# Kernel optimization log

Measured on AMD Instinct MI355X. Metric: run time of the kernel, lower is better.

Reference implementation:

```python
import jax, jax.numpy as jnp
import numpy as np

EPS = 1e-9
# exp factors for iterations i = 4,3,2,1,0,-1,-2 ; i == -2 -> 0.0
EXP_FACTORS = np.array([-(4.0 ** i) if i != -2 else 0.0 for i in range(4, -3, -1)], dtype=np.float32)


def setup_inputs() -> dict:
    key = jax.random.key(0)
    k1, k2 = jax.random.split(key)
    B, N, D = 16, 2048, 256
    preds = jax.random.normal(k1, (B, N, D), dtype=jnp.float32)
    labels = jax.random.normal(k2, (B, N, D), dtype=jnp.float32)
    return {"preds": preds, "labels": labels}


def _pairwise_dist(p1, p2):
    # [B,N,1] + [B,1,N] - 2 * p1 @ p2^T -> [B,N,N]
    p1_norm = jnp.sum(p1 * p1, axis=-1)[..., :, None]
    p2_norm = jnp.sum(p2 * p2, axis=-1)[..., None, :]
    return p1_norm + p2_norm - 2.0 * jnp.einsum('bnd,bmd->bnm', p1, p2)


def _approx_match(pwdist):
    B, N, _ = pwdist.shape
    match0 = jnp.zeros_like(pwdist)
    currency0 = jnp.ones((B, N, 1), dtype=pwdist.dtype)
    cost0 = jnp.ones((B, 1, N), dtype=pwdist.dtype)

    def body(carry, exp_factor):
        match, cost, currency = carry
        bids = jnp.exp(exp_factor * pwdist) * cost              # [B,N,N]
        bids = bids * currency / (jnp.sum(bids, axis=2, keepdims=True) + EPS)
        bid_wt = jnp.minimum(cost / (jnp.sum(bids, axis=1, keepdims=True) + EPS), 1.0)
        bids = bids * bid_wt
        match = match + bids
        cost = jnp.maximum(cost - jnp.sum(bids, axis=1, keepdims=True), 0.0)
        currency = jnp.maximum(currency - jnp.sum(bids, axis=2, keepdims=True), 0.0)
        return (match, cost, currency), None

    (match, _, _), _ = jax.lax.scan(body, (match0, cost0, currency0), jnp.asarray(EXP_FACTORS))
    return match


def reference(preds, labels):
    pwdist = _pairwise_dist(preds, labels)
    match = _approx_match(pwdist)
    return jnp.sum(match * pwdist)
```

## Files before the change

### kernel.cpp

```cpp
#include <hip/hip_runtime.h>
#include <cstdint>

#define B_ 16
#define N_ 2048
#define D_ 256
#define EPS_ 1e-9f

#define AS1 __attribute__((address_space(1)))
#define AS3 __attribute__((address_space(3)))

typedef float f4 __attribute__((ext_vector_type(4)));
typedef __attribute__((ext_vector_type(8))) short short8;

__device__ inline unsigned short f2bf(float x){
  unsigned int u = __float_as_uint(x);
  u = (u + 0x7fffu + ((u >> 16) & 1u)) >> 16;
  return (unsigned short)u;
}
__device__ inline float bf2f(unsigned short u){
  return __uint_as_float(((unsigned int)u) << 16);
}

__device__ float blockReduceSum(float x, float* red){
  int tid = threadIdx.x;
  red[tid] = x; __syncthreads();
  #pragma unroll
  for (int off = 128; off > 0; off >>= 1){
    if (tid < off) red[tid] += red[tid + off];
    __syncthreads();
  }
  float r = red[0]; __syncthreads();
  return r;
}

__global__ __launch_bounds__(256) void prep_kernel(
    const float* __restrict__ preds, const float* __restrict__ labels,
    unsigned short* __restrict__ pabf, unsigned short* __restrict__ pbbf,
    float* __restrict__ pn, float* __restrict__ ln,
    float* __restrict__ cost, float* __restrict__ currency,
    int* __restrict__ dmin, float* __restrict__ PL,
    float* __restrict__ scal, float* __restrict__ out){
  int s = blockIdx.y;
  int tid = threadIdx.x;
  if (s == 0){
    int i = blockIdx.x * 256 + tid;
    if (i < B_ * N_){ cost[i] = 1.f; currency[i] = 1.f; }
    if (i < 2 * B_ * D_) PL[i] = 0.f;
    if (i < B_ * 4) scal[i] = 0.f;
    if (i < B_) dmin[i] = 0x7f7fffff;
    if (i == 0) out[0] = 0.f;
  }
  const float* src = s ? labels : preds;
  unsigned short* dst = s ? pbbf : pabf;
  float* norms = s ? ln : pn;
  int wid = (blockIdx.x * 256 + tid) >> 6;
  int lane = tid & 63;
  size_t row0 = (size_t)wid * 4;
  float4 v[4];
  #pragma unroll
  for (int q = 0; q < 4; q++)
    v[q] = ((const float4*)(src + (row0 + q) * D_))[lane];
  #pragma unroll
  for (int q = 0; q < 4; q++){
    float sum = v[q].x*v[q].x + v[q].y*v[q].y + v[q].z*v[q].z + v[q].w*v[q].w;
    #pragma unroll
    for (int off = 32; off >= 1; off >>= 1) sum += __shfl_xor(sum, off);
    if (lane == 0) norms[row0 + q] = sum;
    ushort4 o; o.x = f2bf(v[q].x); o.y = f2bf(v[q].y); o.z = f2bf(v[q].z); o.w = f2bf(v[q].w);
    ((ushort4*)(dst + (row0 + q) * D_))[lane] = o;
  }
}

__global__ __launch_bounds__(512) void gemm_minmax(
    const unsigned short* __restrict__ pa, const unsigned short* __restrict__ pbm,
    const float* __restrict__ pn, const float* __restrict__ ln,
    int* __restrict__ dmin)
{
  int lid = blockIdx.x;
  int xcd = lid & 7, sq = lid >> 3;
  int b = 2 * xcd + (sq >> 4);
  int rest = sq & 15;
  int tm = (rest >> 1) * 256;
  int tnh = rest & 1;
  const unsigned short* A  = pa  + (size_t)b * N_ * D_;
  const unsigned short* Bm = pbm + (size_t)b * N_ * D_;
  __shared__ __align__(16) unsigned short As[2][256 * 64];
  __shared__ __align__(16) unsigned short Bs[2][256 * 64];
  __shared__ float minred[8];
  int tid = threadIdx.x, lane = tid & 63, w = tid >> 6;
  int wm = (w >> 2) * 128, wn = (w & 3) * 64;
  int quad = lane >> 4, l15 = lane & 15;

  f4 acc[8][4];
  #pragma unroll
  for (int i = 0; i < 8; i++)
    #pragma unroll
    for (int j = 0; j < 4; j++) acc[i][j] = (f4)0.f;

  int lr = lane >> 3, ch = lane & 7;
  int gch = (ch ^ lr) * 8;

  auto load_stage = [&](int st){
    int ti = st >> 2, ki = st & 3;
    int tn = (tnh * 4 + ti) * 256;
    int kt = ki * 64;
    int bufI = st & 1;
    #pragma unroll
    for (int p = 0; p < 4; p++){
      int R = p * 64 + w * 8;
      int r = R + lr;
      __builtin_amdgcn_global_load_lds(
          (const AS1 unsigned int*)(const void*)&A[(size_t)(tm + r) * D_ + kt + gch],
          (AS3 unsigned int*)(void*)&As[bufI][R * 64], 16, 0, 0);
      __builtin_amdgcn_global_load_lds(
          (const AS1 unsigned int*)(const void*)&Bm[(size_t)(tn + r) * D_ + kt + gch],
          (AS3 unsigned int*)(void*)&Bs[bufI][R * 64], 16, 0, 0);
    }
  };

  load_stage(0);
  float lnr[4];
  float mind = 3.4e38f;
  for (int st = 0; st < 16; st++){
    __syncthreads();
    if (st < 15) load_stage(st + 1);
    int ki = st & 3;
    if (ki == 0){
      int tn = (tnh * 4 + (st >> 2)) * 256;
      #pragma unroll
      for (int jj = 0; jj < 4; jj++)
        lnr[jj] = ln[(size_t)b * N_ + tn + wn + jj * 16 + l15];
    }
    int buf = st & 1;
    #pragma unroll
    for (int ks = 0; ks < 2; ks++){
      short8 af[8], bf[4];
      int j = ks * 4 + quad;
      #pragma unroll
      for (int i = 0; i < 8; i++){
        int ra = wm + i * 16 + l15;
        af[i] = *(const short8*)(&As[buf][ra * 64 + ((j ^ (ra & 7)) * 8)]);
      }
      #pragma unroll
      for (int jj = 0; jj < 4; jj++){
        int rb = wn + jj * 16 + l15;
        bf[jj] = *(const short8*)(&Bs[buf][rb * 64 + ((j ^ (rb & 7)) * 8)]);
      }
      #pragma unroll
      for (int i = 0; i < 8; i++)
        #pragma unroll
        for (int jj = 0; jj < 4; jj++)
          acc[i][jj] = __builtin_amdgcn_mfma_f32_16x16x32_bf16(af[i], bf[jj], acc[i][jj], 0, 0, 0);
    }
    if (ki == 3){
      #pragma unroll
      for (int i = 0; i < 8; i++){
        float4 pv4 = *(const float4*)&pn[(size_t)b * N_ + tm + wm + i * 16 + quad * 4];
        float pv[4] = {pv4.x, pv4.y, pv4.z, pv4.w};
        #pragma unroll
        for (int jj = 0; jj < 4; jj++){
          #pragma unroll
          for (int reg = 0; reg < 4; reg++){
            float v = pv[reg] + lnr[jj] - 2.f * acc[i][jj][reg];
            mind = fminf(mind, v);
            acc[i][jj][reg] = 0.f;
          }
        }
      }
    }
  }

  #pragma unroll
  for (int off = 32; off >= 1; off >>= 1) mind = fminf(mind, __shfl_xor(mind, off));
  if (lane == 0) minred[w] = mind;
  __syncthreads();
  if (tid == 0){
    float m = minred[0];
    #pragma unroll
    for (int q = 1; q < 8; q++) m = fminf(m, minred[q]);
    atomicMin(&dmin[b], __float_as_int(fmaxf(m, 0.f)));
  }
}

__global__ __launch_bounds__(256) void fb_all(
    const unsigned short* __restrict__ pabf, const unsigned short* __restrict__ pbbf,
    const float* __restrict__ pn, const float* __restrict__ ln,
    float* __restrict__ cost, float* __restrict__ currency,
    const int* __restrict__ dmin, float* __restrict__ out,
    float* __restrict__ alpha, float* __restrict__ v, float* __restrict__ scal)
{
  const float EF[6] = {-256.f, -64.f, -16.f, -4.f, -1.f, -0.25f};
  int b = blockIdx.x, tid = threadIdx.x;
  float dm = __int_as_float(dmin[b]);
  __shared__ float red[256];
  __shared__ float alpha_l[N_];
  __shared__ float prow[D_];
  const unsigned short* A  = pabf + (size_t)b * N_ * D_;
  const unsigned short* Bm = pbbf + (size_t)b * N_ * D_;
  const float* pnb = pn + (size_t)b * N_;
  const float* lnb = ln + (size_t)b * N_;
  float* costb = cost + (size_t)b * N_;
  float* curb  = currency + (size_t)b * N_;
  for (int it = 0; it < 6; it++){
    float ef = EF[it];
    if (ef * (dm - 8.f) < -55.f) continue;
    float cost_c[8], colsum_c[8], bw_c[8], costnew_c[8];
    #pragma unroll
    for (int j = 0; j < 8; j++){ cost_c[j] = costb[j*256+tid]; colsum_c[j] = 0.f; }
    for (int r = 0; r < N_; r++){
      prow[tid] = bf2f(A[(size_t)r * D_ + tid]);
      __syncthreads();
      float s_c[8], rs = 0.f;
      for (int j = 0; j < 8; j++){
        int m = j*256+tid; float dot = 0.f;
        for (int k = 0; k < D_; k++) dot += prow[k] * bf2f(Bm[(size_t)m * D_ + k]);
        float d = pnb[r] + lnb[m] - 2.f*dot;
        float s = __expf(ef * d) * cost_c[j];
        s_c[j] = s; rs += s;
      }
      float tot = blockReduceSum(rs, red);
      float a = curb[r] / (tot + EPS_);
      if (tid == 0) alpha_l[r] = a;
      #pragma unroll
      for (int j = 0; j < 8; j++) colsum_c[j] += s_c[j] * a;
      __syncthreads();
    }
    #pragma unroll
    for (int j = 0; j < 8; j++){
      float cs = colsum_c[j];
      float bw = fminf(cost_c[j] / (cs + EPS_), 1.f);
      bw_c[j] = bw; costnew_c[j] = fmaxf(cost_c[j] - bw*cs, 0.f);
    }
    float contrib = 0.f;
    for (int r = 0; r < N_; r++){
      prow[tid] = bf2f(A[(size_t)r * D_ + tid]);
      __syncthreads();
      float a = alpha_l[r], rbs = 0.f;
      for (int j = 0; j < 8; j++){
        int m = j*256+tid; float dot = 0.f;
        for (int k = 0; k < D_; k++) dot += prow[k] * bf2f(Bm[(size_t)m * D_ + k]);
        float d = pnb[r] + lnb[m] - 2.f*dot;
        float bid = __expf(ef * d) * cost_c[j] * a * bw_c[j];
        rbs += bid; contrib += bid * d;
      }
      float tot = blockReduceSum(rbs, red);
      if (tid == 0) curb[r] = fmaxf(curb[r] - tot, 0.f);
      __syncthreads();
    }
    #pragma unroll
    for (int j = 0; j < 8; j++) costb[j*256+tid] = costnew_c[j];
    float ctot = blockReduceSum(contrib, red);
    if (tid == 0) atomicAdd(out, ctot);
    __syncthreads();
  }
  float* ab = alpha + (size_t)b * N_;
  float* vb = v + (size_t)b * N_;
  float s = 0.f;
  #pragma unroll
  for (int j = 0; j < 8; j++) s += costb[j*256+tid];
  float Sc = blockReduceSum(s, red);
  float sa = 0.f, spn = 0.f;
  #pragma unroll
  for (int j = 0; j < 8; j++){
    int i = j*256+tid;
    float a = curb[i] / (Sc + EPS_);
    ab[i] = a; sa += a; spn += a * pnb[i];
  }
  float Sa  = blockReduceSum(sa, red);
  float Spn = blockReduceSum(spn, red);
  float sv = 0.f, sln = 0.f;
  #pragma unroll
  for (int j = 0; j < 8; j++){
    int i = j*256+tid;
    float c = costb[j*256+tid];
    float bw = fminf(c / (c * Sa + EPS_), 1.f);
    float vv = c * bw;
    vb[i] = vv; sv += vv; sln += vv * lnb[i];
  }
  float Sv  = blockReduceSum(sv, red);
  float Sln = blockReduceSum(sln, red);
  if (tid == 0){
    scal[b*4+0] = Sa; scal[b*4+1] = Sv; scal[b*4+2] = Spn; scal[b*4+3] = Sln;
  }
}

__global__ __launch_bounds__(256) void cf_wsum(
    const unsigned short* __restrict__ pabf, const unsigned short* __restrict__ pbbf,
    const float* __restrict__ alpha, const float* __restrict__ v,
    float* __restrict__ PL)
{
  int chunk = blockIdx.x, src = blockIdx.y, b = blockIdx.z, tid = threadIdx.x;
  int g = tid >> 6, c4 = (tid & 63) * 4;
  const unsigned short* X = (src ? pbbf : pabf) + ((size_t)b * N_ + chunk * 64) * D_;
  const float* wv = (src ? v : alpha) + (size_t)b * N_ + chunk * 64;
  __shared__ float wl[64];
  __shared__ float part[4][D_];
  if (tid < 64) wl[tid] = wv[tid];
  __syncthreads();
  f4 acc = (f4)0.f;
  for (int r = g * 16; r < g * 16 + 16; r++){
    uint2 pk = *(const uint2*)&X[(size_t)r * D_ + c4];
    float wr = wl[r];
    acc[0] = fmaf(wr, __uint_as_float(pk.x << 16), acc[0]);
    acc[1] = fmaf(wr, __uint_as_float(pk.x & 0xffff0000u), acc[1]);
    acc[2] = fmaf(wr, __uint_as_float(pk.y << 16), acc[2]);
    acc[3] = fmaf(wr, __uint_as_float(pk.y & 0xffff0000u), acc[3]);
  }
  #pragma unroll
  for (int q = 0; q < 4; q++) part[g][c4 + q] = acc[q];
  __syncthreads();
  float s = part[0][tid] + part[1][tid] + part[2][tid] + part[3][tid];
  atomicAdd(&PL[((size_t)src * B_ + b) * D_ + tid], s);
}

__global__ __launch_bounds__(256) void cf_final(
    const float* __restrict__ PL, const float* __restrict__ scal,
    float* __restrict__ out)
{
  int b = blockIdx.x, tid = threadIdx.x;
  __shared__ float red[256];
  float p = PL[(size_t)b * D_ + tid] * PL[((size_t)B_ + b) * D_ + tid];
  float dot = blockReduceSum(p, red);
  if (tid == 0){
    float Sa = scal[b*4+0], Sv = scal[b*4+1], Spn = scal[b*4+2], Sln = scal[b*4+3];
    atomicAdd(out, Spn * Sv + Sa * Sln - 2.f * dot);
  }
}

extern "C" void kernel_launch(void* const* d_in, const int* in_sizes, int n_in,
                              void* d_out, int out_size, void* d_ws, size_t ws_size,
                              hipStream_t stream)
{
  const float* preds  = (const float*)d_in[0];
  const float* labels = (const float*)d_in[1];
  float* out = (float*)d_out;
  char* ws = (char*)d_ws;
  const size_t BN = (size_t)B_ * N_;
  size_t off = 0;
  float* cost     = (float*)(ws + off); off += BN * 4;
  float* currency = (float*)(ws + off); off += BN * 4;
  float* alpha    = (float*)(ws + off); off += BN * 4;
  float* v        = (float*)(ws + off); off += BN * 4;
  float* pn       = (float*)(ws + off); off += BN * 4;
  float* ln       = (float*)(ws + off); off += BN * 4;
  int*   dmin     = (int*)(ws + off);   off += 256;
  float* scal     = (float*)(ws + off); off += 256;
  float* PL       = (float*)(ws + off); off += (size_t)2 * B_ * D_ * 4;
  unsigned short* pabf = (unsigned short*)(ws + off); off += BN * D_ * 2;
  unsigned short* pbbf = (unsigned short*)(ws + off); off += BN * D_ * 2;

  prep_kernel<<<dim3((unsigned)(BN / 16), 2), 256, 0, stream>>>(
      preds, labels, pabf, pbbf, pn, ln, cost, currency, dmin, PL, scal, out);
  gemm_minmax<<<dim3(256), 512, 0, stream>>>(pabf, pbbf, pn, ln, dmin);
  fb_all<<<dim3(B_), 256, 0, stream>>>(pabf, pbbf, pn, ln, cost, currency, dmin, out,
                                       alpha, v, scal);
  cf_wsum<<<dim3(32, 2, B_), 256, 0, stream>>>(pabf, pbbf, alpha, v, PL);
  cf_final<<<dim3(B_), 256, 0, stream>>>(PL, scal, out);
}
```

Measured before the change: 152.4 us.

## Retile min-distance GEMM into smaller 256x128 tiles across more blocks

Retiles the pairwise-distance min-reduction GEMM from 256 persistent blocks, each sweeping four 256x256 output tiles, to 2048 blocks that each own one 256x128 tile with K-steps of 32. The LDS layout is reswizzled to pack two 32-wide rows per 64-element line, and the accumulator array is halved so up to four blocks can be resident per CU. This aims to raise occupancy and latency hiding on a GEMM that left most CUs underused. In exchange, operands are reloaded more often and there are more block launches and atomics.

Measured after the change: 157.1 us. 1.03x slower.

```diff
diff --git a/kernel.cpp b/kernel.cpp
--- a/kernel.cpp
+++ b/kernel.cpp
@@ -71,105 +71,108 @@
   }
 }
 
-__global__ __launch_bounds__(512) void gemm_minmax(
+__global__ __launch_bounds__(512, 4) void gemm_minmax(
     const unsigned short* __restrict__ pa, const unsigned short* __restrict__ pbm,
     const float* __restrict__ pn, const float* __restrict__ ln,
     int* __restrict__ dmin)
 {
   int lid = blockIdx.x;
   int xcd = lid & 7, sq = lid >> 3;
-  int b = 2 * xcd + (sq >> 4);
-  int rest = sq & 15;
-  int tm = (rest >> 1) * 256;
-  int tnh = rest & 1;
+  int b = 2 * xcd + (sq >> 7);
+  int t = sq & 127;
+  int tm = (t & 7) * 256;
+  int tn = (t >> 3) * 128;
   const unsigned short* A  = pa  + (size_t)b * N_ * D_;
   const unsigned short* Bm = pbm + (size_t)b * N_ * D_;
-  __shared__ __align__(16) unsigned short As[2][256 * 64];
-  __shared__ __align__(16) unsigned short Bs[2][256 * 64];
+  __shared__ __align__(16) unsigned short As[2][256 * 32];
+  __shared__ __align__(16) unsigned short Bs[2][128 * 32];
   __shared__ float minred[8];
   int tid = threadIdx.x, lane = tid & 63, w = tid >> 6;
-  int wm = (w >> 2) * 128, wn = (w & 3) * 64;
+  int wm = (w >> 1) * 64, wn = (w & 1) * 64;
   int quad = lane >> 4, l15 = lane & 15;
-
-  f4 acc[8][4];
-  #pragma unroll
-  for (int i = 0; i < 8; i++)
+  int l8 = lane >> 3, c7 = lane & 7;
+
+  f4 acc[4][4];
+  #pragma unroll
+  for (int i = 0; i < 4; i++)
     #pragma unroll
     for (int j = 0; j < 4; j++) acc[i][j] = (f4)0.f;
 
-  int lr = lane >> 3, ch = lane & 7;
-  int gch = (ch ^ lr) * 8;
-
-  auto load_stage = [&](int st){
-    int ti = st >> 2, ki = st & 3;
-    int tn = (tnh * 4 + ti) * 256;
-    int kt = ki * 64;
-    int bufI = st & 1;
-    #pragma unroll
-    for (int p = 0; p < 4; p++){
-      int R = p * 64 + w * 8;
-      int r = R + lr;
+  auto stage = [&](int ki, int bufI){
+    int kt = ki * 32;
+    #pragma unroll
+    for (int p = 0; p < 2; p++){
+      int Q0 = p * 64 + w * 8;
+      int q = Q0 + l8;
+      int c = c7 ^ (q & 7);
+      int sr = 2 * q + (c >> 2);
+      int kc = c & 3;
       __builtin_amdgcn_global_load_lds(
-          (const AS1 unsigned int*)(const void*)&A[(size_t)(tm + r) * D_ + kt + gch],
-          (AS3 unsigned int*)(void*)&As[bufI][R * 64], 16, 0, 0);
+          (const AS1 unsigned int*)(const void*)&A[(size_t)(tm + sr) * D_ + kt + kc * 8],
+          (AS3 unsigned int*)(void*)&As[bufI][Q0 * 64], 16, 0, 0);
+    }
+    {
+      int Q0 = w * 8;
+      int q = Q0 + l8;
+      int c = c7 ^ (q & 7);
+      int sr = 2 * q + (c >> 2);
+      int kc = c & 3;
       __builtin_amdgcn_global_load_lds(
-          (const AS1 unsigned int*)(const void*)&Bm[(size_t)(tn + r) * D_ + kt + gch],
-          (AS3 unsigned int*)(void*)&Bs[bufI][R * 64], 16, 0, 0);
+          (const AS1 unsigned int*)(const void*)&Bm[(size_t)(tn + sr) * D_ + kt + kc * 8],
+          (AS3 unsigned int*)(void*)&Bs[bufI][Q0 * 64], 16, 0, 0);
     }
   };
 
-  load_stage(0);
-  float lnr[4];
-  float mind = 3.4e38f;
-  for (int st = 0; st < 16; st++){
+  stage(0, 0);
+  int buf = 0;
+  for (int ki = 0; ki < 8; ki++){
     __syncthreads();
-    if (st < 15) load_stage(st + 1);
-    int ki = st & 3;
-    if (ki == 0){
-      int tn = (tnh * 4 + (st >> 2)) * 256;
+    if (ki < 7) stage(ki + 1, buf ^ 1);
+    short8 af[4], bf[4];
+    #pragma unroll
+    for (int i = 0; i < 4; i++){
+      int ra = wm + i * 16 + l15;
+      int q = ra >> 1;
+      int c = (ra & 1) * 4 + quad;
+      af[i] = *(const short8*)(&As[buf][q * 64 + ((c ^ (q & 7)) * 8)]);
+    }
+    #pragma unroll
+    for (int jj = 0; jj < 4; jj++){
+      int rb = wn + jj * 16 + l15;
+      int q = rb >> 1;
+      int c = (rb & 1) * 4 + quad;
+      bf[jj] = *(const short8*)(&Bs[buf][q * 64 + ((c ^ (q & 7)) * 8)]);
+    }
+    #pragma unroll
+    for (int i = 0; i < 4; i++)
       #pragma unroll
       for (int jj = 0; jj < 4; jj++)
-        lnr[jj] = ln[(size_t)b * N_ + tn + wn + jj * 16 + l15];
-    }
-    int buf = st & 1;
-    #pragma unroll
-    for (int ks = 0; ks < 2; ks++){
-      short8 af[8], bf[4];
-      int j = ks * 4 + quad;
+        acc[i][jj] = __builtin_amdgcn_mfma_f32_16x16x32_bf16(af[i], bf[jj], acc[i][jj], 0, 0, 0);
+    buf ^= 1;
+  }
+
+  float4 pnr[4];
+  float lnr[4];
+  #pragma unroll
+  for (int i = 0; i < 4; i++)
+    pnr[i] = *(const float4*)&pn[(size_t)b * N_ + tm + wm + i * 16 + quad * 4];
+  #pragma unroll
+  for (int jj = 0; jj < 4; jj++)
+    lnr[jj] = ln[(size_t)b * N_ + tn + wn + jj * 16 + l15];
+
+  float mind = 3.4e38f;
+  #pragma unroll
+  for (int i = 0; i < 4; i++){
+    float pv[4] = {pnr[i].x, pnr[i].y, pnr[i].z, pnr[i].w};
+    #pragma unroll
+    for (int jj = 0; jj < 4; jj++){
       #pragma unroll
-      for (int i = 0; i < 8; i++){
-        int ra = wm + i * 16 + l15;
-        af[i] = *(const short8*)(&As[buf][ra * 64 + ((j ^ (ra & 7)) * 8)]);
+      for (int reg = 0; reg < 4; reg++){
+        float v = pv[reg] + lnr[jj] - 2.f * acc[i][jj][reg];
+        mind = fminf(mind, v);
       }
-      #pragma unroll
-      for (int jj = 0; jj < 4; jj++){
-        int rb = wn + jj * 16 + l15;
-        bf[jj] = *(const short8*)(&Bs[buf][rb * 64 + ((j ^ (rb & 7)) * 8)]);
-      }
-      #pragma unroll
-      for (int i = 0; i < 8; i++)
-        #pragma unroll
-        for (int jj = 0; jj < 4; jj++)
-          acc[i][jj] = __builtin_amdgcn_mfma_f32_16x16x32_bf16(af[i], bf[jj], acc[i][jj], 0, 0, 0);
-    }
-    if (ki == 3){
-      #pragma unroll
-      for (int i = 0; i < 8; i++){
-        float4 pv4 = *(const float4*)&pn[(size_t)b * N_ + tm + wm + i * 16 + quad * 4];
-        float pv[4] = {pv4.x, pv4.y, pv4.z, pv4.w};
-        #pragma unroll
-        for (int jj = 0; jj < 4; jj++){
-          #pragma unroll
-          for (int reg = 0; reg < 4; reg++){
-            float v = pv[reg] + lnr[jj] - 2.f * acc[i][jj][reg];
-            mind = fminf(mind, v);
-            acc[i][jj][reg] = 0.f;
-          }
-        }
-      }
-    }
-  }
-
+    }
+  }
   #pragma unroll
   for (int off = 32; off >= 1; off >>= 1) mind = fminf(mind, __shfl_xor(mind, off));
   if (lane == 0) minred[w] = mind;
@@ -351,7 +354,7 @@
 
   prep_kernel<<<dim3((unsigned)(BN / 16), 2), 256, 0, stream>>>(
       preds, labels, pabf, pbbf, pn, ln, cost, currency, dmin, PL, scal, out);
-  gemm_minmax<<<dim3(256), 512, 0, stream>>>(pabf, pbbf, pn, ln, dmin);
+  gemm_minmax<<<dim3(2048), 512, 0, stream>>>(pabf, pbbf, pn, ln, dmin);
   fb_all<<<dim3(B_), 256, 0, stream>>>(pabf, pbbf, pn, ln, cost, currency, dmin, out,
                                        alpha, v, scal);
   cf_wsum<<<dim3(32, 2, B_), 256, 0, stream>>>(pabf, pbbf, alpha, v, PL);
```
